# Optimization experiments

Hardware: AMD Instinct MI355X
Metric: run time of the kernel (lower is better)

Reference implementation:

```python
import jax, jax.numpy as jnp
import numpy as np
from itertools import combinations

SPARSITY = 2
MARGIN = 0.1
N = 96   # sample_size
D = 64   # sample_dim


def setup_inputs() -> dict:
    key = jax.random.key(0)
    k1, k2 = jax.random.split(key)
    # labels in {-1, +1} (forward() uses labels directly as multiplicative signs)
    labels = jnp.where(jax.random.uniform(k1, (N,)) < 0.5, -1.0, 1.0).astype(jnp.float32)
    features = jax.random.normal(k2, (N, D), dtype=jnp.float32)
    # torch.combinations(arange(N), k) equivalents (static index tables)
    sample_idx = jnp.asarray(np.array(list(combinations(range(N), SPARSITY)), dtype=np.int32))  # [Ms, k]
    feat_idx = jnp.asarray(np.array(list(combinations(range(D), SPARSITY)), dtype=np.int32))    # [Mf, k]
    return {"labels": labels, "features": features,
            "sample_idx": sample_idx, "feat_idx": feat_idx}


def reference(labels, features, sample_idx, feat_idx):
    Ms, k = sample_idx.shape
    Mf = feat_idx.shape[0]
    # labeled_features = labels.unsqueeze(1) * features
    lf = labels[:, None] * features                      # [N, D]
    # gather sample combinations then feature combinations:
    # M[(f, s), i, j] = lf[sample_idx[s, i], feat_idx[f, j]]
    G = lf[sample_idx]                                   # [Ms, k, D]
    M = G[:, :, feat_idx]                                # [Ms, k, Mf, k]
    M = jnp.transpose(M, (2, 0, 1, 3)).reshape(Mf * Ms, k, k)
    # label combinations repeated across feature combos, minus margin
    y = jnp.tile(labels[sample_idx], (Mf, 1)) - MARGIN   # [Mf*Ms, k]
    # batched tiny pinv solve: w = pinv(M) @ (y - margin)
    weights = jnp.squeeze(jnp.linalg.pinv(M) @ y[..., None], -1)  # [Mf*Ms, k]
    # sparse COO column indices for each weight row (rows are 0..batch-1 per slice)
    col_indices = jnp.repeat(feat_idx, Ms, axis=0)       # [Mf*Ms, k]
    return weights, col_indices
```

## Files before the change

kernel.cpp:

```cpp
#include <hip/hip_runtime.h>
#include <math.h>


#define NSAMP 96
#define NFEAT 64
#define MS 4560
#define MF 2016
#define TOTAL (MS * MF)
#define RCOND 2.384185791015625e-06
#define RC2 (RCOND * RCOND)
#define RC2F ((float)RC2)
#define BANDHI 1.00001f
#define BANDLO 0.99999f

typedef float f32x4 __attribute__((ext_vector_type(4)));

__global__ __launch_bounds__(256) void prep_kernel(
    const float* __restrict__ labels,
    const float* __restrict__ features,
    float* __restrict__ lfT)
{
    int t = blockIdx.x * blockDim.x + threadIdx.x;
    if (t >= NSAMP * NFEAT) return;
    int a = t / NSAMP;
    int i = t - a * NSAMP;
    lfT[t] = labels[i] * features[i * NFEAT + a];
}

__device__ __forceinline__ void solve2x2(
    float a00, float a01, float a10, float a11,
    float li, float lj, float& w0, float& w1)
{
    float p    = a01 * a10;
    float e    = fmaf(a01, a10, -p);
    float detk = fmaf(a00, a11, -p) + e;

    float fr = fmaf(a11, a11, fmaf(a10, a10, fmaf(a01, a01, a00 * a00)));
    float d2 = detk * detk;
    float rc = RC2F * fr * fr;

    bool full;
    if (d2 > rc * BANDHI) {
        full = true;
    } else if (d2 < rc * BANDLO) {
        full = false;
    } else {
        double dA00 = (double)a00, dA01 = (double)a01;
        double dA10 = (double)a10, dA11 = (double)a11;
        double det = dA00 * dA11 - dA01 * dA10;
        double dfr = dA00 * dA00 + dA01 * dA01 + dA10 * dA10 + dA11 * dA11;
        full = det * det > RC2 * (dfr * dfr);
    }

    float y0 = li - 0.1f, y1 = lj - 0.1f;
    if (full) {
        float rd   = 1.0f / detk;
        float num0 = fmaf(a11, y0, -(a01 * y1));
        float num1 = fmaf(a00, y1, -(a10 * y0));
        w0 = num0 * rd;
        w1 = num1 * rd;
    } else {
        if (fr > 0.0f) {
            float rf = 1.0f / fr;
            w0 = fmaf(a00, y0, a10 * y1) * rf;
            w1 = fmaf(a01, y0, a11 * y1) * rf;
        } else {
            w0 = 0.0f;
            w1 = 0.0f;
        }
    }
}

__global__ __launch_bounds__(256) void rll_kernel(
    const float* __restrict__ labels,
    const float* __restrict__ lfT,
    const int*   __restrict__ sample_idx,
    const int*   __restrict__ feat_idx,
    float* __restrict__ w_out,
    float* __restrict__ c_out)
{
    int t = blockIdx.x * blockDim.x + threadIdx.x;
    if (t >= MS / 2) return;
    int f = blockIdx.y;

    int2 ab = ((const int2*)feat_idx)[f];
    const float* __restrict__ rowA = lfT + ab.x * NSAMP;
    const float* __restrict__ rowB = lfT + ab.y * NSAMP;

    int4 ss = ((const int4*)sample_idx)[t];

    float li0 = labels[ss.x], lj0 = labels[ss.y];
    float w00, w01;
    solve2x2(rowA[ss.x], rowB[ss.x], rowA[ss.y], rowB[ss.y], li0, lj0, w00, w01);
    float li1 = labels[ss.z], lj1 = labels[ss.w];
    float w10, w11;
    solve2x2(rowA[ss.z], rowB[ss.z], rowA[ss.w], rowB[ss.w], li1, lj1, w10, w11);

    size_t q = (size_t)f * (MS / 2) + t;
    f32x4 wv = { w00, w01, w10, w11 };
    __builtin_nontemporal_store(wv, (f32x4*)w_out + q);
    float af = (float)ab.x, bf = (float)ab.y;
    f32x4 cv = { af, bf, af, bf };
    __builtin_nontemporal_store(cv, (f32x4*)c_out + q);
}

extern "C" void kernel_launch(void* const* d_in, const int* in_sizes, int n_in,
                              void* d_out, int out_size, void* d_ws, size_t ws_size,
                              hipStream_t stream) {
    const float* labels     = (const float*)d_in[0];
    const float* features   = (const float*)d_in[1];
    const int*   sample_idx = (const int*)d_in[2];
    const int*   feat_idx   = (const int*)d_in[3];

    float* lfT   = (float*)d_ws;
    float* w_out = (float*)d_out;
    float* c_out = (float*)d_out + (size_t)TOTAL * 2;

    prep_kernel<<<(NSAMP * NFEAT + 255) / 256, 256, 0, stream>>>(
        labels, features, lfT);

    dim3 grid((MS / 2 + 255) / 256, MF);
    rll_kernel<<<grid, 256, 0, stream>>>(labels, lfT, sample_idx,
                                         feat_idx, w_out, c_out);
}
```

Measured before the change: 35.70 us.

## Process four sample pairs per thread and precompute shifted labels

Each thread now solves four 2x2 systems, taken from two halves of the sample-pair range, instead of two, using 128-thread blocks. The label-minus-margin values are precomputed into the workspace by the prep kernel, and divisions use the hardware reciprocal. The aim is more ILP and amortised index loads per thread. The trade-offs are slightly reduced reciprocal precision and fewer threads in flight for a store-bound kernel.

```diff
diff --git a/kernel.cpp b/kernel.cpp
--- a/kernel.cpp
+++ b/kernel.cpp
@@ -7,6 +7,7 @@
 #define MS 4560
 #define MF 2016
 #define TOTAL (MS * MF)
+#define QT (MS / 4)
 #define RCOND 2.384185791015625e-06
 #define RC2 (RCOND * RCOND)
 #define RC2F ((float)RC2)
@@ -21,15 +22,19 @@
     float* __restrict__ lfT)
 {
     int t = blockIdx.x * blockDim.x + threadIdx.x;
-    if (t >= NSAMP * NFEAT) return;
-    int a = t / NSAMP;
-    int i = t - a * NSAMP;
-    lfT[t] = labels[i] * features[i * NFEAT + a];
+    if (t < NSAMP * NFEAT) {
+        int a = t / NSAMP;
+        int i = t - a * NSAMP;
+        lfT[t] = labels[i] * features[i * NFEAT + a];
+    } else if (t < NSAMP * NFEAT + NSAMP) {
+        int i = t - NSAMP * NFEAT;
+        lfT[t] = labels[i] - 0.1f;
+    }
 }
 
 __device__ __forceinline__ void solve2x2(
     float a00, float a01, float a10, float a11,
-    float li, float lj, float& w0, float& w1)
+    float y0, float y1, float& w0, float& w1)
 {
     float p    = a01 * a10;
     float e    = fmaf(a01, a10, -p);
@@ -52,16 +57,15 @@
         full = det * det > RC2 * (dfr * dfr);
     }
 
-    float y0 = li - 0.1f, y1 = lj - 0.1f;
     if (full) {
-        float rd   = 1.0f / detk;
+        float rd   = __builtin_amdgcn_rcpf(detk);
         float num0 = fmaf(a11, y0, -(a01 * y1));
         float num1 = fmaf(a00, y1, -(a10 * y0));
         w0 = num0 * rd;
         w1 = num1 * rd;
     } else {
         if (fr > 0.0f) {
-            float rf = 1.0f / fr;
+            float rf = __builtin_amdgcn_rcpf(fr);
             w0 = fmaf(a00, y0, a10 * y1) * rf;
             w1 = fmaf(a01, y0, a11 * y1) * rf;
         } else {
@@ -71,8 +75,7 @@
     }
 }
 
-__global__ __launch_bounds__(256) void rll_kernel(
-    const float* __restrict__ labels,
+__global__ __launch_bounds__(128, 8) void rll_kernel(
     const float* __restrict__ lfT,
     const int*   __restrict__ sample_idx,
     const int*   __restrict__ feat_idx,
@@ -80,28 +83,39 @@
     float* __restrict__ c_out)
 {
     int t = blockIdx.x * blockDim.x + threadIdx.x;
-    if (t >= MS / 2) return;
+    if (t >= QT) return;
     int f = blockIdx.y;
 
     int2 ab = ((const int2*)feat_idx)[f];
     const float* __restrict__ rowA = lfT + ab.x * NSAMP;
     const float* __restrict__ rowB = lfT + ab.y * NSAMP;
+    const float* __restrict__ yv   = lfT + NSAMP * NFEAT;
 
-    int4 ss = ((const int4*)sample_idx)[t];
+    int4 s1 = ((const int4*)sample_idx)[t];
+    int4 s2 = ((const int4*)sample_idx)[t + QT];
 
-    float li0 = labels[ss.x], lj0 = labels[ss.y];
-    float w00, w01;
-    solve2x2(rowA[ss.x], rowB[ss.x], rowA[ss.y], rowB[ss.y], li0, lj0, w00, w01);
-    float li1 = labels[ss.z], lj1 = labels[ss.w];
-    float w10, w11;
-    solve2x2(rowA[ss.z], rowB[ss.z], rowA[ss.w], rowB[ss.w], li1, lj1, w10, w11);
+    float aA0 = rowA[s1.x], aB0 = rowB[s1.x], aA0j = rowA[s1.y], aB0j = rowB[s1.y];
+    float aA1 = rowA[s1.z], aB1 = rowB[s1.z], aA1j = rowA[s1.w], aB1j = rowB[s1.w];
+    float aA2 = rowA[s2.x], aB2 = rowB[s2.x], aA2j = rowA[s2.y], aB2j = rowB[s2.y];
+    float aA3 = rowA[s2.z], aB3 = rowB[s2.z], aA3j = rowA[s2.w], aB3j = rowB[s2.w];
+    float y00 = yv[s1.x], y01 = yv[s1.y], y10 = yv[s1.z], y11 = yv[s1.w];
+    float y20 = yv[s2.x], y21 = yv[s2.y], y30 = yv[s2.z], y31 = yv[s2.w];
+
+    float w00, w01, w10, w11, w20, w21, w30, w31;
+    solve2x2(aA0, aB0, aA0j, aB0j, y00, y01, w00, w01);
+    solve2x2(aA1, aB1, aA1j, aB1j, y10, y11, w10, w11);
+    solve2x2(aA2, aB2, aA2j, aB2j, y20, y21, w20, w21);
+    solve2x2(aA3, aB3, aA3j, aB3j, y30, y31, w30, w31);
 
     size_t q = (size_t)f * (MS / 2) + t;
-    f32x4 wv = { w00, w01, w10, w11 };
-    __builtin_nontemporal_store(wv, (f32x4*)w_out + q);
+    f32x4 wv1 = { w00, w01, w10, w11 };
+    f32x4 wv2 = { w20, w21, w30, w31 };
+    __builtin_nontemporal_store(wv1, (f32x4*)w_out + q);
+    __builtin_nontemporal_store(wv2, (f32x4*)w_out + q + QT);
     float af = (float)ab.x, bf = (float)ab.y;
     f32x4 cv = { af, bf, af, bf };
     __builtin_nontemporal_store(cv, (f32x4*)c_out + q);
+    __builtin_nontemporal_store(cv, (f32x4*)c_out + q + QT);
 }
 
 extern "C" void kernel_launch(void* const* d_in, const int* in_sizes, int n_in,
@@ -116,10 +130,10 @@
     float* w_out = (float*)d_out;
     float* c_out = (float*)d_out + (size_t)TOTAL * 2;
 
-    prep_kernel<<<(NSAMP * NFEAT + 255) / 256, 256, 0, stream>>>(
+    prep_kernel<<<(NSAMP * NFEAT + NSAMP + 255) / 256, 256, 0, stream>>>(
         labels, features, lfT);
 
-    dim3 grid((MS / 2 + 255) / 256, MF);
-    rll_kernel<<<grid, 256, 0, stream>>>(labels, lfT, sample_idx,
-                                         feat_idx, w_out, c_out);
+    dim3 grid((QT + 127) / 128, MF);
+    rll_kernel<<<grid, 128, 0, stream>>>(lfT, sample_idx, feat_idx,
+                                         w_out, c_out);
 }
```

New measurement: 36.39 us. Within noise of the previous version (+1.9%).

## Fuse prep into solver via shared-memory staging, use fast reciprocal, drop nontemporal stores

Applied to the files above, without the earlier changes.

Removes the separate prep kernel. Each block now loads the two needed feature columns and the shifted labels into shared memory, and gathers the 2x2 matrix entries from LDS instead of global memory. It also swaps the IEEE divisions for the hardware rcp approximation and replaces the nontemporal vector stores with plain stores. This saves one launch and the gathered global loads. In exchange every block does redundant staging work plus a barrier, and rcp may differ slightly in precision from true division.

```diff
diff --git a/kernel.cpp b/kernel.cpp
--- a/kernel.cpp
+++ b/kernel.cpp
@@ -6,7 +6,7 @@
 #define NFEAT 64
 #define MS 4560
 #define MF 2016
-#define TOTAL (MS * MF)
+#define HT (MS / 2)
 #define RCOND 2.384185791015625e-06
 #define RC2 (RCOND * RCOND)
 #define RC2F ((float)RC2)
@@ -15,21 +15,9 @@
 
 typedef float f32x4 __attribute__((ext_vector_type(4)));
 
-__global__ __launch_bounds__(256) void prep_kernel(
-    const float* __restrict__ labels,
-    const float* __restrict__ features,
-    float* __restrict__ lfT)
-{
-    int t = blockIdx.x * blockDim.x + threadIdx.x;
-    if (t >= NSAMP * NFEAT) return;
-    int a = t / NSAMP;
-    int i = t - a * NSAMP;
-    lfT[t] = labels[i] * features[i * NFEAT + a];
-}
-
 __device__ __forceinline__ void solve2x2(
     float a00, float a01, float a10, float a11,
-    float li, float lj, float& w0, float& w1)
+    float y0, float y1, float& w0, float& w1)
 {
     float p    = a01 * a10;
     float e    = fmaf(a01, a10, -p);
@@ -52,16 +40,13 @@
         full = det * det > RC2 * (dfr * dfr);
     }
 
-    float y0 = li - 0.1f, y1 = lj - 0.1f;
     if (full) {
-        float rd   = 1.0f / detk;
-        float num0 = fmaf(a11, y0, -(a01 * y1));
-        float num1 = fmaf(a00, y1, -(a10 * y0));
-        w0 = num0 * rd;
-        w1 = num1 * rd;
+        float rd   = __builtin_amdgcn_rcpf(detk);
+        w0 = fmaf(a11, y0, -(a01 * y1)) * rd;
+        w1 = fmaf(a00, y1, -(a10 * y0)) * rd;
     } else {
         if (fr > 0.0f) {
-            float rf = 1.0f / fr;
+            float rf = __builtin_amdgcn_rcpf(fr);
             w0 = fmaf(a00, y0, a10 * y1) * rf;
             w1 = fmaf(a01, y0, a11 * y1) * rf;
         } else {
@@ -73,35 +58,45 @@
 
 __global__ __launch_bounds__(256) void rll_kernel(
     const float* __restrict__ labels,
-    const float* __restrict__ lfT,
+    const float* __restrict__ features,
     const int*   __restrict__ sample_idx,
     const int*   __restrict__ feat_idx,
     float* __restrict__ w_out,
     float* __restrict__ c_out)
 {
-    int t = blockIdx.x * blockDim.x + threadIdx.x;
-    if (t >= MS / 2) return;
+    __shared__ float sA[NSAMP];
+    __shared__ float sB[NSAMP];
+    __shared__ float sY[NSAMP];
+
     int f = blockIdx.y;
+    int2 ab = ((const int2*)feat_idx)[f];
+    int tid = threadIdx.x;
 
-    int2 ab = ((const int2*)feat_idx)[f];
-    const float* __restrict__ rowA = lfT + ab.x * NSAMP;
-    const float* __restrict__ rowB = lfT + ab.y * NSAMP;
+    if (tid < NSAMP) {
+        float l = labels[tid];
+        sY[tid] = l - 0.1f;
+        sA[tid] = l * features[tid * NFEAT + ab.x];
+        sB[tid] = l * features[tid * NFEAT + ab.y];
+    }
+    __syncthreads();
+
+    int t = blockIdx.x * blockDim.x + tid;
+    if (t >= HT) return;
 
     int4 ss = ((const int4*)sample_idx)[t];
 
-    float li0 = labels[ss.x], lj0 = labels[ss.y];
-    float w00, w01;
-    solve2x2(rowA[ss.x], rowB[ss.x], rowA[ss.y], rowB[ss.y], li0, lj0, w00, w01);
-    float li1 = labels[ss.z], lj1 = labels[ss.w];
-    float w10, w11;
-    solve2x2(rowA[ss.z], rowB[ss.z], rowA[ss.w], rowB[ss.w], li1, lj1, w10, w11);
+    float w00, w01, w10, w11;
+    solve2x2(sA[ss.x], sB[ss.x], sA[ss.y], sB[ss.y], sY[ss.x], sY[ss.y],
+             w00, w01);
+    solve2x2(sA[ss.z], sB[ss.z], sA[ss.w], sB[ss.w], sY[ss.z], sY[ss.w],
+             w10, w11);
 
-    size_t q = (size_t)f * (MS / 2) + t;
+    size_t q = (size_t)f * HT + t;
     f32x4 wv = { w00, w01, w10, w11 };
-    __builtin_nontemporal_store(wv, (f32x4*)w_out + q);
+    *((f32x4*)w_out + q) = wv;
     float af = (float)ab.x, bf = (float)ab.y;
     f32x4 cv = { af, bf, af, bf };
-    __builtin_nontemporal_store(cv, (f32x4*)c_out + q);
+    *((f32x4*)c_out + q) = cv;
 }
 
 extern "C" void kernel_launch(void* const* d_in, const int* in_sizes, int n_in,
@@ -112,14 +107,10 @@
     const int*   sample_idx = (const int*)d_in[2];
     const int*   feat_idx   = (const int*)d_in[3];
 
-    float* lfT   = (float*)d_ws;
     float* w_out = (float*)d_out;
-    float* c_out = (float*)d_out + (size_t)TOTAL * 2;
+    float* c_out = (float*)d_out + (size_t)MS * MF * 2;
 
-    prep_kernel<<<(NSAMP * NFEAT + 255) / 256, 256, 0, stream>>>(
-        labels, features, lfT);
-
-    dim3 grid((MS / 2 + 255) / 256, MF);
-    rll_kernel<<<grid, 256, 0, stream>>>(labels, lfT, sample_idx,
+    dim3 grid((HT + 255) / 256, MF);
+    rll_kernel<<<grid, 256, 0, stream>>>(labels, features, sample_idx,
                                          feat_idx, w_out, c_out);
 }
```

After: 30.34 us. 1.18x faster.
